# Performance work log

Hardware: AMD Instinct MI355X
Metric: run time of the kernel (lower is better)

The kernel has to match this reference:

```python
import jax, jax.numpy as jnp
import numpy as np

NEG_SLOPE = 0.2
EPS = 1e-16  # PyG softmax denominator epsilon


def setup_inputs() -> dict:
    key = jax.random.key(0)
    k1, k2, k3, k4 = jax.random.split(key, 4)
    N, E, F_in, F_out = 50000, 800000, 256, 128
    x = jax.random.normal(k1, (N, F_in), dtype=jnp.float32)
    edge_index = jax.random.randint(k2, (2, E), 0, N, dtype=jnp.int64)
    # Glorot-ish scaled params (values irrelevant to correctness, scale keeps softmax sane)
    W = jax.random.normal(k3, (F_in, F_out), dtype=jnp.float32) * (1.0 / np.sqrt(F_in))
    ka, kb = jax.random.split(k4)
    att_src = jax.random.normal(ka, (F_out,), dtype=jnp.float32) * (1.0 / np.sqrt(F_out))
    att_dst = jax.random.normal(kb, (F_out,), dtype=jnp.float32) * (1.0 / np.sqrt(F_out))
    bias = jnp.zeros((F_out,), dtype=jnp.float32)
    return {"x": x, "edge_index": edge_index, "W": W, "att_src": att_src, "att_dst": att_dst, "bias": bias}


def reference(x, edge_index, W, att_src, att_dst, bias):
    N = x.shape[0]
    # Linear transform (no bias in PyG GATConv's lin)
    h = x @ W  # [N, F_out]
    # Add self loops (GATConv default add_self_loops=True)
    loops = jnp.arange(N, dtype=edge_index.dtype)
    src = jnp.concatenate([edge_index[0], loops])  # [E+N]
    dst = jnp.concatenate([edge_index[1], loops])
    # Per-node attention logits, gathered per edge
    a_src = h @ att_src  # [N]
    a_dst = h @ att_dst  # [N]
    e = jax.nn.leaky_relu(a_src[src] + a_dst[dst], NEG_SLOPE)  # [E+N]
    # Segment softmax over incoming edges of each destination node
    e_max = jax.ops.segment_max(e, dst, num_segments=N)  # every segment nonempty (self loops)
    e_exp = jnp.exp(e - e_max[dst])
    denom = jax.ops.segment_sum(e_exp, dst, num_segments=N)
    alpha = e_exp / (denom[dst] + EPS)  # [E+N]
    # Scatter-aggregate weighted source features
    out = jax.ops.segment_sum(alpha[:, None] * h[src], dst, num_segments=N)  # [N, F_out]
    return out + bias
```

## Files before the change

### kernel.cpp

```cpp
#include <hip/hip_runtime.h>
#include <cstdint>
#include <cstddef>

#define F_IN 256
#define F_OUT 128
#define NEG_SLOPE 0.2f
#define NPB 64
#define MAXBUK 1024
#define BCAP 2048
#define EPB 4096
#define WT_STRIDE 72

typedef short short8 __attribute__((ext_vector_type(8)));
typedef float f32x4 __attribute__((ext_vector_type(4)));

__device__ __forceinline__ unsigned short f2bf_rne(float f) {
  unsigned u = __float_as_uint(f);
  u += 0x7FFFu + ((u >> 16) & 1u);
  return (unsigned short)(u >> 16);
}

__device__ __forceinline__ float bf_lo(unsigned u) { return __uint_as_float(u << 16); }
__device__ __forceinline__ float bf_hi(unsigned u) { return __uint_as_float(u & 0xFFFF0000u); }

__global__ __launch_bounds__(256) void setup_kernel(const float* __restrict__ W,
                                                    unsigned short* __restrict__ Wt,
                                                    int* __restrict__ bucketcnt, int nbuk) {
  int idx = blockIdx.x * 256 + threadIdx.x;
  if (idx < F_IN * F_OUT) {
    int n = idx & 127, k = idx >> 7;
    Wt[(size_t)n * F_IN + k] = f2bf_rne(W[(size_t)k * F_OUT + n]);
  }
  if (idx < nbuk) bucketcnt[idx] = 0;
}

__global__ __launch_bounds__(256, 4) void gemm_build_kernel(
    const float* __restrict__ x, const unsigned short* __restrict__ Wt,
    const float* __restrict__ att_src, const float* __restrict__ att_dst,
    unsigned short* __restrict__ hb, float* __restrict__ a_src, float* __restrict__ a_dst,
    int N, const int* __restrict__ ei, int* __restrict__ bucketcnt,
    unsigned* __restrict__ csrw, int E, int nbuk, int buildBlocks) {
  __shared__ __attribute__((aligned(16))) char lds_raw[128 * WT_STRIDE * 2];
  const int tid = threadIdx.x;

  if ((int)blockIdx.x < buildBlocks) {
    int* lhist = (int*)lds_raw;
    int* gbase = (int*)(lds_raw + 4096);
    const int e0 = blockIdx.x * EPB;
    for (int i = tid; i < nbuk; i += 256) lhist[i] = 0;
    __syncthreads();
    int lr[16], lb[16];
    unsigned lw[16];
#pragma unroll
    for (int i = 0; i < 16; ++i) {
      int e = e0 + i * 256 + tid;
      lb[i] = -1;
      if (e < E) {
        int s = ei[e], d = ei[E + e];
        lb[i] = d >> 6;
        lw[i] = ((unsigned)(d & 63) << 26) | (unsigned)s;
        lr[i] = atomicAdd(&lhist[lb[i]], 1);
      }
    }
    __syncthreads();
    for (int i = tid; i < nbuk; i += 256) {
      int c = lhist[i];
      if (c > 0) gbase[i] = atomicAdd(&bucketcnt[i], c);
    }
    __syncthreads();
#pragma unroll
    for (int i = 0; i < 16; ++i) {
      if (lb[i] >= 0) {
        int off = gbase[lb[i]] + lr[i];
        if (off < BCAP) csrw[(size_t)lb[i] * BCAP + off] = lw[i];
      }
    }
    return;
  }

  unsigned short* wt_l = (unsigned short*)lds_raw;
  const int bid  = blockIdx.x - buildBlocks;
  const int lane = tid & 63;
  const int wv   = tid >> 6;
  const int q    = lane >> 4;
  const int l16  = lane & 15;
  const int m0   = bid * 64;
  const int m    = m0 + wv * 16 + l16;
  const int mc   = (m < N) ? m : (N - 1);

  f32x4 acc[8];
#pragma unroll
  for (int i = 0; i < 8; ++i) acc[i] = (f32x4)(0.f);

  const int srow  = tid >> 1;
  const int shalf = tid & 1;

#pragma unroll 1
  for (int t = 0; t < 4; ++t) {
    {
      const unsigned short* g = Wt + (size_t)srow * F_IN + t * 64 + shalf * 32;
      unsigned short* l = wt_l + srow * WT_STRIDE + shalf * 32;
#pragma unroll
      for (int j = 0; j < 4; ++j)
        *(uint4*)(l + j * 8) = *(const uint4*)(g + j * 8);
    }
    __syncthreads();

#pragma unroll
    for (int s = 0; s < 2; ++s) {
      const int kg = t * 64 + s * 32 + q * 8;
      f32x4 a0 = *(const f32x4*)(x + (size_t)mc * F_IN + kg);
      f32x4 a1 = *(const f32x4*)(x + (size_t)mc * F_IN + kg + 4);
      short8 av;
      av[0] = (short)f2bf_rne(a0[0]); av[1] = (short)f2bf_rne(a0[1]);
      av[2] = (short)f2bf_rne(a0[2]); av[3] = (short)f2bf_rne(a0[3]);
      av[4] = (short)f2bf_rne(a1[0]); av[5] = (short)f2bf_rne(a1[1]);
      av[6] = (short)f2bf_rne(a1[2]); av[7] = (short)f2bf_rne(a1[3]);
#pragma unroll
      for (int nt = 0; nt < 8; ++nt) {
        short8 bv = *(const short8*)(wt_l + (nt * 16 + l16) * WT_STRIDE + s * 32 + q * 8);
        acc[nt] = __builtin_amdgcn_mfma_f32_16x16x32_bf16(av, bv, acc[nt], 0, 0, 0);
      }
    }
    __syncthreads();
  }

  float as_c[8], ad_c[8];
#pragma unroll
  for (int nt = 0; nt < 8; ++nt) {
    as_c[nt] = att_src[nt * 16 + l16];
    ad_c[nt] = att_dst[nt * 16 + l16];
  }
  float ps[4] = {0.f, 0.f, 0.f, 0.f}, pd[4] = {0.f, 0.f, 0.f, 0.f};
#pragma unroll
  for (int nt = 0; nt < 8; ++nt)
#pragma unroll
    for (int r = 0; r < 4; ++r) {
      ps[r] += acc[nt][r] * as_c[nt];
      pd[r] += acc[nt][r] * ad_c[nt];
    }
#pragma unroll
  for (int r = 0; r < 4; ++r) {
    int gm = m0 + wv * 16 + q * 4 + r;
    if (gm < N) {
#pragma unroll
      for (int nt = 0; nt < 8; ++nt)
        hb[(size_t)gm * F_OUT + nt * 16 + l16] = f2bf_rne(acc[nt][r]);
    }
  }
#pragma unroll
  for (int r = 0; r < 4; ++r) {
#pragma unroll
    for (int off = 1; off <= 8; off <<= 1) {
      ps[r] += __shfl_xor(ps[r], off, 64);
      pd[r] += __shfl_xor(pd[r], off, 64);
    }
  }
  if (l16 == 0) {
#pragma unroll
    for (int r = 0; r < 4; ++r) {
      int gm = m0 + wv * 16 + q * 4 + r;
      if (gm < N) { a_src[gm] = ps[r]; a_dst[gm] = pd[r]; }
    }
  }
}

__global__ __launch_bounds__(256) void aggregate_kernel(const unsigned short* __restrict__ hb,
                                                        const unsigned* __restrict__ csrw,
                                                        const float* __restrict__ a_src,
                                                        const float* __restrict__ a_dst,
                                                        const int* __restrict__ bucketcnt,
                                                        const float* __restrict__ bias,
                                                        float* __restrict__ out, int N) {
  __shared__ unsigned sw[BCAP];
  __shared__ unsigned sorted[BCAP + NPB];
  __shared__ int start[NPB + 1];
  __shared__ int fill[NPB];
  __shared__ float adl[NPB];
  const int tid = threadIdx.x;
  const int n0  = blockIdx.x * NPB;
  int cnt = bucketcnt[blockIdx.x];
  cnt = (cnt < BCAP) ? cnt : BCAP;

  if (tid < NPB) {
    int n = n0 + tid;
    start[1 + tid] = (n < N) ? 1 : 0;
    fill[tid] = 1;
    adl[tid] = (n < N) ? a_dst[n] : 0.f;
  }
  __syncthreads();
  for (int j = tid; j < cnt; j += 256) {
    unsigned w = csrw[(size_t)blockIdx.x * BCAP + j];
    sw[j] = w;
    atomicAdd(&start[1 + (int)(w >> 26)], 1);
  }
  __syncthreads();
  if (tid < NPB) {
    int incl = start[1 + tid];
#pragma unroll
    for (int off = 1; off < NPB; off <<= 1) {
      int t = __shfl_up(incl, off, 64);
      if (tid >= off) incl += t;
    }
    start[1 + tid] = incl;
    if (tid == 0) start[0] = 0;
  }
  __syncthreads();
  if (tid < NPB && n0 + tid < N)
    sorted[start[tid]] = ((unsigned)tid << 26) | (unsigned)(n0 + tid);
  for (int j = tid; j < cnt; j += 256) {
    unsigned w = sw[j];
    int loc = (int)(w >> 26);
    sorted[start[loc] + atomicAdd(&fill[loc], 1)] = w;
  }
  __syncthreads();

  const int g   = tid >> 4;
  const int l16 = tid & 15;
  const unsigned short* hrow = hb + l16 * 8;
  const float4 bb0 = *(const float4*)(bias + l16 * 8);
  const float4 bb1 = *(const float4*)(bias + l16 * 8 + 4);
#pragma unroll 1
  for (int r = 0; r < 4; ++r) {
    int loc = g + r * 16;
    int n = n0 + loc;
    if (n >= N) continue;
    int b0 = start[loc], b1 = start[loc + 1];
    f32x4 acc0 = (f32x4)(0.f), acc1 = (f32x4)(0.f);
    float s = 0.f;
    for (int jb = b0; jb < b1; jb += 8) {
      int jj = jb + (l16 & 7);
      float p = 0.f;
      int c = 0;
      if (jj < b1) {
        unsigned w = sorted[jj];
        c = (int)(w & 0x03FFFFFFu);
        float e = a_src[c] + adl[loc];
        e = (e > 0.f) ? e : NEG_SLOPE * e;
        p = __expf(e);
      }
      s += (l16 < 8) ? p : 0.f;
#pragma unroll
      for (int k = 0; k < 8; ++k) {
        float pk = __shfl(p, k, 8);
        int   ck = __shfl(c, k, 8);
        const uint4 hv = *(const uint4*)(hrow + (size_t)ck * F_OUT);
        acc0[0] += pk * bf_lo(hv.x); acc0[1] += pk * bf_hi(hv.x);
        acc0[2] += pk * bf_lo(hv.y); acc0[3] += pk * bf_hi(hv.y);
        acc1[0] += pk * bf_lo(hv.z); acc1[1] += pk * bf_hi(hv.z);
        acc1[2] += pk * bf_lo(hv.w); acc1[3] += pk * bf_hi(hv.w);
      }
    }
#pragma unroll
    for (int off = 1; off < 16; off <<= 1) s += __shfl_xor(s, off, 16);

    float sc = 1.f / (s + 1e-16f);
    float4 o0, o1;
    o0.x = acc0[0] * sc + bb0.x;
    o0.y = acc0[1] * sc + bb0.y;
    o0.z = acc0[2] * sc + bb0.z;
    o0.w = acc0[3] * sc + bb0.w;
    o1.x = acc1[0] * sc + bb1.x;
    o1.y = acc1[1] * sc + bb1.y;
    o1.z = acc1[2] * sc + bb1.z;
    o1.w = acc1[3] * sc + bb1.w;
    *(float4*)&out[(size_t)n * F_OUT + l16 * 8]     = o0;
    *(float4*)&out[(size_t)n * F_OUT + l16 * 8 + 4] = o1;
  }
}

extern "C" void kernel_launch(void* const* d_in, const int* in_sizes, int n_in,
                              void* d_out, int out_size, void* d_ws, size_t ws_size,
                              hipStream_t stream) {
  const float* x     = (const float*)d_in[0];
  const int*   ei    = (const int*)d_in[1];
  const float* W     = (const float*)d_in[2];
  const float* att_s = (const float*)d_in[3];
  const float* att_d = (const float*)d_in[4];
  const float* bias  = (const float*)d_in[5];
  float* out = (float*)d_out;

  const int N = in_sizes[0] / F_IN;
  const int E = in_sizes[1] / 2;
  const int nbuk = (N + NPB - 1) / NPB;
  const int gemmBlocks  = (N + 63) / 64;
  const int buildBlocks = (E + EPB - 1) / EPB;

  char* p = (char*)d_ws;
  unsigned short* wt = (unsigned short*)p; p += (size_t)F_IN * F_OUT * sizeof(unsigned short);
  unsigned short* hb = (unsigned short*)p; p += (size_t)N * F_OUT * sizeof(unsigned short);
  float* a_src = (float*)p;  p += (size_t)N * sizeof(float);
  float* a_dst = (float*)p;  p += (size_t)N * sizeof(float);
  int*   bcnt  = (int*)p;    p += (size_t)nbuk * sizeof(int);
  p = (char*)(((uintptr_t)p + 15) & ~(uintptr_t)15);
  unsigned* csrw = (unsigned*)p; p += (size_t)nbuk * BCAP * sizeof(unsigned);

  int setup_n = (F_IN * F_OUT > nbuk) ? F_IN * F_OUT : nbuk;
  setup_kernel<<<(setup_n + 255) / 256, 256, 0, stream>>>(W, wt, bcnt, nbuk);
  gemm_build_kernel<<<buildBlocks + gemmBlocks, 256, 0, stream>>>(
      x, wt, att_s, att_d, hb, a_src, a_dst, N, ei, bcnt, csrw, E, nbuk, buildBlocks);
  aggregate_kernel<<<nbuk, 256, 0, stream>>>(hb, csrw, a_src, a_dst, bcnt, bias, out, N);
}
```

Measured before the change: 147.6 us.

## Locally sort edges by bucket in LDS before writing to global buckets

The build blocks now compute a prefix sum over the per-block bucket histogram, scatter edge words into LDS sorted by bucket, then have each thread copy one bucket's contiguous run to global memory. This replaces scattered per-edge global writes with runs of consecutive stores per bucket, aiming for better write coalescing. The cost is extra LDS (the shared array grows), an extra scan with its barriers, and serial per-thread copy loops that are poorly coalesced across lanes, since each lane writes a different bucket. The copy loop's work is also unbalanced across threads.

```diff
diff --git a/kernel.cpp b/kernel.cpp
--- a/kernel.cpp
+++ b/kernel.cpp
@@ -40,14 +40,17 @@
     unsigned short* __restrict__ hb, float* __restrict__ a_src, float* __restrict__ a_dst,
     int N, const int* __restrict__ ei, int* __restrict__ bucketcnt,
     unsigned* __restrict__ csrw, int E, int nbuk, int buildBlocks) {
-  __shared__ __attribute__((aligned(16))) char lds_raw[128 * WT_STRIDE * 2];
+  __shared__ __attribute__((aligned(16))) char lds_raw[3 * 4096 + EPB * 4 + 32];
   const int tid = threadIdx.x;
 
   if ((int)blockIdx.x < buildBlocks) {
-    int* lhist = (int*)lds_raw;
-    int* gbase = (int*)(lds_raw + 4096);
+    int*      lhist   = (int*)lds_raw;
+    int*      lstart  = (int*)(lds_raw + 4096);
+    int*      gbase   = (int*)(lds_raw + 8192);
+    unsigned* sortedw = (unsigned*)(lds_raw + 12288);
+    int*      wsumB   = (int*)(lds_raw + 12288 + EPB * 4);
     const int e0 = blockIdx.x * EPB;
-    for (int i = tid; i < nbuk; i += 256) lhist[i] = 0;
+    for (int i = tid; i < MAXBUK; i += 256) lhist[i] = 0;
     __syncthreads();
     int lr[16], lb[16];
     unsigned lw[16];
@@ -63,16 +66,51 @@
       }
     }
     __syncthreads();
+    {
+      const int lane = tid & 63, wid = tid >> 6;
+      int c[4];
+      int s = 0;
+#pragma unroll
+      for (int qq = 0; qq < 4; ++qq) {
+        c[qq] = lhist[tid * 4 + qq];
+        s += c[qq];
+      }
+      int incl = s;
+#pragma unroll
+      for (int off = 1; off < 64; off <<= 1) {
+        int t = __shfl_up(incl, off, 64);
+        if (lane >= off) incl += t;
+      }
+      if (lane == 63) wsumB[wid] = incl;
+      __syncthreads();
+      int woff = 0;
+#pragma unroll
+      for (int w = 0; w < 4; ++w)
+        if (w < wid) woff += wsumB[w];
+      int base = woff + incl - s;
+#pragma unroll
+      for (int qq = 0; qq < 4; ++qq) {
+        lstart[tid * 4 + qq] = base;
+        base += c[qq];
+      }
+    }
+    __syncthreads();
+#pragma unroll
+    for (int i = 0; i < 16; ++i)
+      if (lb[i] >= 0) sortedw[lstart[lb[i]] + lr[i]] = lw[i];
     for (int i = tid; i < nbuk; i += 256) {
       int c = lhist[i];
       if (c > 0) gbase[i] = atomicAdd(&bucketcnt[i], c);
     }
     __syncthreads();
-#pragma unroll
-    for (int i = 0; i < 16; ++i) {
-      if (lb[i] >= 0) {
-        int off = gbase[lb[i]] + lr[i];
-        if (off < BCAP) csrw[(size_t)lb[i] * BCAP + off] = lw[i];
+    for (int b = tid; b < nbuk; b += 256) {
+      int c = lhist[b];
+      if (c == 0) continue;
+      int gb = gbase[b], ls = lstart[b];
+      unsigned* dst = csrw + (size_t)b * BCAP;
+      for (int k = 0; k < c; ++k) {
+        int off = gb + k;
+        if (off < BCAP) dst[off] = sortedw[ls + k];
       }
     }
     return;
```

New measurement: 150.7 us. +2.1%, slower.
